# Performance work log

Measured on AMD Instinct MI355X. Metric: run time of the kernel, lower is better.

The kernel has to match this reference:

```python
import jax, jax.numpy as jnp
import numpy as np

ROPE_THETA = 10000.0

def _rope(x, offset=0):
    # x: [B, H, T, d]; lucidrains rotary_embedding_torch interleaved-pair convention
    d = x.shape[-1]
    T = x.shape[-2]
    inv_freq = 1.0 / (ROPE_THETA ** (jnp.arange(0, d, 2, dtype=jnp.float32) / d))  # [d/2]
    t = jnp.arange(offset, offset + T, dtype=jnp.float32)
    freqs = t[:, None] * inv_freq[None, :]                 # [T, d/2]
    freqs = jnp.repeat(freqs, 2, axis=-1)                  # [T, d] (each freq duplicated for its pair)
    cos = jnp.cos(freqs).astype(x.dtype)
    sin = jnp.sin(freqs).astype(x.dtype)
    xr = x.reshape(*x.shape[:-1], d // 2, 2)
    x1, x2 = xr[..., 0], xr[..., 1]
    rot = jnp.stack([-x2, x1], axis=-1).reshape(x.shape)   # rotate_half, interleaved
    return x * cos + rot * sin


def setup_inputs() -> dict:
    key = jax.random.key(0)
    ks = jax.random.split(key, 5)
    B, T, C = 8, 1024, 1024
    s = 0.02
    x = jax.random.normal(ks[0], (B, T, C), dtype=jnp.float32)
    ipw = jax.random.normal(ks[1], (3 * C, C), dtype=jnp.float32) * s
    ipb = jax.random.normal(ks[2], (3 * C,), dtype=jnp.float32) * s
    opw = jax.random.normal(ks[3], (C, C), dtype=jnp.float32) * s
    opb = jax.random.normal(ks[4], (C,), dtype=jnp.float32) * s
    # bool mask, True = blocked (original code inverts before SDPA) -> causal
    causal_block = ~jnp.tril(jnp.ones((T, T), dtype=bool))
    attn_mask = causal_block[None, None, :, :]             # [1,1,T,T]
    return {"x": x, "ipw": ipw, "ipb": ipb, "opw": opw, "opb": opb,
            "attn_mask": attn_mask}


def reference(x, ipw, ipb, opw, opb, attn_mask):
    B, T, C = x.shape
    n_head = 16
    hd = C // n_head
    qkv = x @ ipw.T + ipb                                  # [B,T,3C]
    q, k, v = jnp.split(qkv, 3, axis=-1)
    def heads(z):
        return z.reshape(B, T, n_head, hd).transpose(0, 2, 1, 3)  # [B,H,T,hd]
    q, k, v = heads(q), heads(k), heads(v)
    q = _rope(q)
    k = _rope(k)
    scores = jnp.einsum('bhqd,bhkd->bhqk', q, k) / jnp.sqrt(jnp.asarray(hd, x.dtype))
    # attn_mask True = blocked; mask slice [FULL_T-T:FULL_T, :FULL_T] is the full mask here
    scores = jnp.where(attn_mask, jnp.asarray(-1e9, x.dtype), scores)
    attn = jax.nn.softmax(scores, axis=-1)
    y = jnp.einsum('bhqk,bhkd->bhqd', attn, v)             # [B,H,T,hd]
    y = y.transpose(0, 2, 1, 3).reshape(B, T, C)
    return y @ opw.T + opb
```

## Files before the change

### kernel.cpp

```cpp
#include <hip/hip_runtime.h>
#include <stdint.h>


typedef __bf16 bf16x8 __attribute__((ext_vector_type(8)));
typedef float f32x4 __attribute__((ext_vector_type(4)));
typedef __attribute__((address_space(1))) unsigned int as1_u32;
typedef __attribute__((address_space(3))) unsigned int as3_u32;

#define MFMA16(a, b, c) __builtin_amdgcn_mfma_f32_16x16x32_bf16((a), (b), (c), 0, 0, 0)

static __device__ __forceinline__ unsigned short f2bf(float f) {
    union { float f; unsigned u; } x; x.f = f;
    return (unsigned short)((x.u + 0x7fffu + ((x.u >> 16) & 1u)) >> 16);
}
static __device__ __forceinline__ float bf2f(unsigned short u) {
    union { unsigned u; float f; } x; x.u = ((unsigned)u) << 16;
    return x.f;
}
static __device__ __forceinline__ bf16x8 ld_bf16x8(const void* p) {
    return *(const bf16x8*)p;
}
static __device__ __forceinline__ unsigned cvtpk(float lo, float hi) {
    unsigned r;
    asm("v_cvt_pk_bf16_f32 %0, %1, %2" : "=v"(r) : "v"(lo), "v"(hi));
    return r;
}

__global__ void cast_f32_bf16(const float* __restrict__ in,
                              unsigned short* __restrict__ out, int n8) {
    int i = blockIdx.x * blockDim.x + threadIdx.x;
    if (i >= n8) return;
    float4 a = ((const float4*)in)[2 * i];
    float4 b = ((const float4*)in)[2 * i + 1];
    union { unsigned short us[8]; uint4 v; } o;
    o.us[0] = f2bf(a.x); o.us[1] = f2bf(a.y); o.us[2] = f2bf(a.z); o.us[3] = f2bf(a.w);
    o.us[4] = f2bf(b.x); o.us[5] = f2bf(b.y); o.us[6] = f2bf(b.z); o.us[7] = f2bf(b.w);
    ((uint4*)out)[i] = o.v;
}

__global__ void rope_table(float* __restrict__ ct, float* __restrict__ st) {
    int idx = blockIdx.x * blockDim.x + threadIdx.x;
    if (idx >= 1024 * 32) return;
    int t = idx >> 5, i = idx & 31;
    float inv = powf(10000.0f, -(float)(2 * i) * (1.0f / 64.0f));
    float f = (float)t * inv;
    ct[idx] = cosf(f);
    st[idx] = sinf(f);
}

template <int NC, bool OUT_BF16>
__global__ __launch_bounds__(256) void gemm_bt(const unsigned short* __restrict__ A,
                                               const unsigned short* __restrict__ W,
                                               const float* __restrict__ bias,
                                               void* __restrict__ Cout, int K) {
    __shared__ __attribute__((aligned(16))) unsigned short As[128 * 32];
    __shared__ __attribute__((aligned(16))) unsigned short Bs[128 * 32];

    constexpr int NT = NC / 128;
    int nwg = gridDim.x;
    int bid = blockIdx.x;
    int lg = (bid & 7) * (nwg >> 3) + (bid >> 3);
    int tm = lg / NT, tn = lg % NT;
    int m0 = tm * 128, n0 = tn * 128;

    int tid = threadIdx.x;
    int w = tid >> 6, l = tid & 63;
    int lr = l & 15, g = l >> 4;
    int ldsb = __builtin_amdgcn_readfirstlane(w * 512);

    int c0 = tid, c1 = tid + 256;
    const unsigned short* A0 = A + (size_t)(m0 + (c0 >> 2)) * K + (c0 & 3) * 8;
    const unsigned short* A1 = A + (size_t)(m0 + (c1 >> 2)) * K + (c1 & 3) * 8;
    const unsigned short* W0 = W + (size_t)(n0 + (c0 >> 2)) * K + (c0 & 3) * 8;
    const unsigned short* W1 = W + (size_t)(n0 + (c1 >> 2)) * K + (c1 & 3) * 8;

    f32x4 acc[4][4] = {};
    int wr = (w >> 1) * 64, wc = (w & 1) * 64;

    for (int k0 = 0; k0 < K; k0 += 32) {
        __syncthreads();
        __builtin_amdgcn_global_load_lds((const as1_u32*)(A0 + k0), (as3_u32*)(As + ldsb), 16, 0, 0);
        __builtin_amdgcn_global_load_lds((const as1_u32*)(A1 + k0), (as3_u32*)(As + 2048 + ldsb), 16, 0, 0);
        __builtin_amdgcn_global_load_lds((const as1_u32*)(W0 + k0), (as3_u32*)(Bs + ldsb), 16, 0, 0);
        __builtin_amdgcn_global_load_lds((const as1_u32*)(W1 + k0), (as3_u32*)(Bs + 2048 + ldsb), 16, 0, 0);
        __syncthreads();

        bf16x8 a[4], b[4];
#pragma unroll
        for (int i = 0; i < 4; ++i) a[i] = ld_bf16x8(As + (wr + i * 16 + lr) * 32 + g * 8);
#pragma unroll
        for (int j = 0; j < 4; ++j) b[j] = ld_bf16x8(Bs + (wc + j * 16 + lr) * 32 + g * 8);
#pragma unroll
        for (int i = 0; i < 4; ++i)
#pragma unroll
            for (int j = 0; j < 4; ++j) acc[i][j] = MFMA16(a[i], b[j], acc[i][j]);
    }

    int g4 = g * 4;
#pragma unroll
    for (int j = 0; j < 4; ++j) {
        int col = n0 + wc + j * 16 + lr;
        float bv = bias[col];
#pragma unroll
        for (int i = 0; i < 4; ++i) {
#pragma unroll
            for (int r = 0; r < 4; ++r) {
                int row = m0 + wr + i * 16 + g4 + r;
                float v = acc[i][j][r] + bv;
                if (OUT_BF16)
                    ((unsigned short*)Cout)[(size_t)row * NC + col] = f2bf(v);
                else
                    ((float*)Cout)[(size_t)row * NC + col] = v;
            }
        }
    }
}

__global__ void rope_reshape(const unsigned short* __restrict__ qkv,
                             const float* __restrict__ ct, const float* __restrict__ st,
                             unsigned short* __restrict__ Qh,
                             unsigned short* __restrict__ Kh) {
    int idx = blockIdx.x * blockDim.x + threadIdx.x;
    if (idx >= 8192 * 256) return;
    int row = idx >> 8;
    int col = (idx & 255) * 8;
    int sec = col >> 10;
    int wi = col & 1023;
    int h = wi >> 6, d = wi & 63;
    int t = row & 1023;

    uint4 raw = *(const uint4*)(qkv + (size_t)row * 3072 + col);
    size_t obase = ((size_t)((row >> 10) * 16 + h) * 1024 + t) * 64 + d;

    union { uint4 v; unsigned short us[8]; } u; u.v = raw;
    float x[8];
#pragma unroll
    for (int i = 0; i < 8; ++i) x[i] = bf2f(u.us[i]);
    float scale = (sec == 0) ? 0.125f : 1.0f;
    union { uint4 v; unsigned short us[8]; } o;
#pragma unroll
    for (int p = 0; p < 4; ++p) {
        int fi = t * 32 + (d >> 1) + p;
        float c = ct[fi], s = st[fi];
        float e0 = (x[2 * p] * c - x[2 * p + 1] * s) * scale;
        float e1 = (x[2 * p + 1] * c + x[2 * p] * s) * scale;
        o.us[2 * p] = f2bf(e0);
        o.us[2 * p + 1] = f2bf(e1);
    }
    unsigned short* dst = (sec == 0) ? Qh : Kh;
    *(uint4*)(dst + obase) = o.v;
}

__global__ __launch_bounds__(256) void transpose_v(const unsigned short* __restrict__ qkv,
                                                   unsigned short* __restrict__ Vt) {
    __shared__ unsigned short Ts[64 * 67];
    int bid = blockIdx.x;
    int bh = bid >> 4, tt = bid & 15;
    int b = bh >> 4, h = bh & 15;
    int t0 = tt * 64;
    int tid = threadIdx.x;
#pragma unroll
    for (int cc = 0; cc < 2; ++cc) {
        int c = tid + cc * 256;
        int trow = c >> 3, d8 = (c & 7) * 8;
        uint4 v = *(const uint4*)(qkv + (size_t)(b * 1024 + t0 + trow) * 3072 + 2048 + h * 64 + d8);
        union { uint4 v; unsigned short us[8]; } u; u.v = v;
#pragma unroll
        for (int i = 0; i < 8; ++i) Ts[trow * 67 + d8 + i] = u.us[i];
    }
    __syncthreads();
#pragma unroll
    for (int cc = 0; cc < 2; ++cc) {
        int c = tid + cc * 256;
        int drow = c >> 3, t8 = (c & 7) * 8;
        union { uint4 v; unsigned short us[8]; } u;
#pragma unroll
        for (int i = 0; i < 8; ++i) u.us[i] = Ts[(t8 + i) * 67 + drow];
        *(uint4*)(Vt + (size_t)bh * 65536 + (size_t)drow * 1024 + t0 + t8) = u.v;
    }
}

__device__ __forceinline__ void attn_tile(const unsigned short* Ks, const unsigned short* Vs,
                                          bf16x8 q0f, bf16x8 q1f, f32x4 (&y)[4],
                                          float& rm, float& rl,
                                          int lr, int g, bool diag, int wq) {
    const char* kc = (const char*)Ks;
    const char* vc = (const char*)Vs;
    int l7 = lr & 7;
    int kof0 = lr * 128 + ((g ^ l7) << 4);
    int kof1 = lr * 128 + (((g + 4) ^ l7) << 4);
    f32x4 s[4];
#pragma unroll
    for (int nt = 0; nt < 4; ++nt) {
        bf16x8 kf0 = ld_bf16x8(kc + nt * 2048 + kof0);
        bf16x8 kf1 = ld_bf16x8(kc + nt * 2048 + kof1);
        f32x4 z = {};
        z = MFMA16(kf0, q0f, z);
        z = MFMA16(kf1, q1f, z);
        s[nt] = z;
    }
    if (diag) {
#pragma unroll
        for (int nt = 0; nt < 4; ++nt)
#pragma unroll
            for (int r = 0; r < 4; ++r)
                if (nt * 16 + g * 4 + r > wq + lr) s[nt][r] = -3e38f;
    }
    float tm;
    {
        f32x4 m4;
#pragma unroll
        for (int r = 0; r < 4; ++r) m4[r] = fmaxf(fmaxf(s[0][r], s[1][r]), fmaxf(s[2][r], s[3][r]));
        tm = fmaxf(fmaxf(m4[0], m4[1]), fmaxf(m4[2], m4[3]));
    }
    tm = fmaxf(tm, __shfl_xor(tm, 16));
    tm = fmaxf(tm, __shfl_xor(tm, 32));
    float nm = fmaxf(rm, tm);
    float alpha = __expf(rm - nm);
    rm = nm;
    float ts = 0.f;
#pragma unroll
    for (int nt = 0; nt < 4; ++nt)
#pragma unroll
        for (int r = 0; r < 4; ++r) { float pv = __expf(s[nt][r] - nm); s[nt][r] = pv; ts += pv; }
    ts += __shfl_xor(ts, 16);
    ts += __shfl_xor(ts, 32);
    rl = rl * alpha + ts;
#pragma unroll
    for (int nt = 0; nt < 4; ++nt) y[nt] *= alpha;
    union { unsigned u[4]; bf16x8 v; } pf0, pf1;
    pf0.u[0] = cvtpk(s[0][0], s[0][1]); pf0.u[1] = cvtpk(s[0][2], s[0][3]);
    pf0.u[2] = cvtpk(s[1][0], s[1][1]); pf0.u[3] = cvtpk(s[1][2], s[1][3]);
    pf1.u[0] = cvtpk(s[2][0], s[2][1]); pf1.u[1] = cvtpk(s[2][2], s[2][3]);
    pf1.u[2] = cvtpk(s[3][0], s[3][1]); pf1.u[3] = cvtpk(s[3][2], s[3][3]);
    int s0 = g >> 1, h8 = (g & 1) * 8;
    int vo0 = lr * 128 + h8 + (((s0 + 0) ^ l7) << 4);
    int vo1 = lr * 128 + h8 + (((s0 + 2) ^ l7) << 4);
    int vo2 = lr * 128 + h8 + (((s0 + 4) ^ l7) << 4);
    int vo3 = lr * 128 + h8 + (((s0 + 6) ^ l7) << 4);
#pragma unroll
    for (int nt = 0; nt < 4; ++nt) {
        union { uint2 u2[2]; bf16x8 v; } vf;
        vf.u2[0] = *(const uint2*)(vc + nt * 2048 + vo0);
        vf.u2[1] = *(const uint2*)(vc + nt * 2048 + vo1);
        y[nt] = MFMA16(vf.v, pf0.v, y[nt]);
        union { uint2 u2[2]; bf16x8 v; } vg;
        vg.u2[0] = *(const uint2*)(vc + nt * 2048 + vo2);
        vg.u2[1] = *(const uint2*)(vc + nt * 2048 + vo3);
        y[nt] = MFMA16(vg.v, pf1.v, y[nt]);
    }
}

__device__ __forceinline__ void attn_epilogue(unsigned short* smem, unsigned short* __restrict__ Yb,
                                              f32x4 (&y)[4], float rl, int qtile,
                                              int b, int hh, int w, int lr, int g, int tid) {
    __syncthreads();
    float inv = 1.0f / rl;
    char* ep = (char*)smem;
#pragma unroll
    for (int nt = 0; nt < 4; ++nt) {
        uint2 pr;
        pr.x = cvtpk(y[nt][0] * inv, y[nt][1] * inv);
        pr.y = cvtpk(y[nt][2] * inv, y[nt][3] * inv);
        *(uint2*)(ep + (w * 16 + lr) * 144 + (nt * 16 + g * 4) * 2) = pr;
    }
    __syncthreads();
    int q = tid >> 2, dc = (tid & 3) * 16;
    uint4 u0 = *(const uint4*)(ep + q * 144 + dc * 2);
    uint4 u1 = *(const uint4*)(ep + q * 144 + dc * 2 + 16);
    size_t orow = ((size_t)(b * 1024 + qtile * 64 + q)) * 1024 + hh * 64 + dc;
    *(uint4*)(Yb + orow) = u0;
    *(uint4*)(Yb + orow + 8) = u1;
}

__global__ __launch_bounds__(256) void attn_fwd(const unsigned short* __restrict__ Qh,
                                                const unsigned short* __restrict__ Kh,
                                                const unsigned short* __restrict__ Vt,
                                                unsigned short* __restrict__ Yb) {
    __shared__ __attribute__((aligned(16))) unsigned short smem[8192];
    unsigned short* Ks = smem;
    unsigned short* Vs = smem + 4096;

    int bid = blockIdx.x;
    int lg = (bid & 7) * 128 + (bid >> 3);
    int bh = lg >> 3, p = lg & 7;
    int qa = p, qb = 15 - p;

    int tid = threadIdx.x, w = tid >> 6, l = tid & 63;
    int lr = l & 15, g = l >> 4;
    int ldsb = __builtin_amdgcn_readfirstlane(w * 512);

    size_t bh64 = (size_t)bh * 65536;
    const unsigned short* qbase = Qh + bh64 + (size_t)(w * 16 + lr) * 64 + g * 8;
    bf16x8 qA0 = ld_bf16x8(qbase + qa * 4096);
    bf16x8 qA1 = ld_bf16x8(qbase + qa * 4096 + 32);
    bf16x8 qB0 = ld_bf16x8(qbase + qb * 4096);
    bf16x8 qB1 = ld_bf16x8(qbase + qb * 4096 + 32);

    f32x4 yA[4] = {}, yB[4] = {};
    float mA = -3e38f, lA = 0.f, mB = -3e38f, lB = 0.f;

    int c0 = tid, c1 = tid + 256;
    const unsigned short* K0 = Kh + bh64 + (c0 >> 3) * 64 + ((c0 ^ (c0 >> 3)) & 7) * 8;
    const unsigned short* K1 = Kh + bh64 + (c1 >> 3) * 64 + ((c1 ^ (c1 >> 3)) & 7) * 8;
    const unsigned short* V0 = Vt + bh64 + (c0 >> 3) * 1024 + ((c0 ^ (c0 >> 3)) & 7) * 8;
    const unsigned short* V1 = Vt + bh64 + (c1 >> 3) * 1024 + ((c1 ^ (c1 >> 3)) & 7) * 8;

    for (int t = 0; t <= qb; ++t) {
        __syncthreads();
        __builtin_amdgcn_global_load_lds((const as1_u32*)(K0 + t * 4096), (as3_u32*)(Ks + ldsb), 16, 0, 0);
        __builtin_amdgcn_global_load_lds((const as1_u32*)(K1 + t * 4096), (as3_u32*)(Ks + 2048 + ldsb), 16, 0, 0);
        __builtin_amdgcn_global_load_lds((const as1_u32*)(V0 + t * 64), (as3_u32*)(Vs + ldsb), 16, 0, 0);
        __builtin_amdgcn_global_load_lds((const as1_u32*)(V1 + t * 64), (as3_u32*)(Vs + 2048 + ldsb), 16, 0, 0);
        __syncthreads();

        if (t <= qa)
            attn_tile(Ks, Vs, qA0, qA1, yA, mA, lA, lr, g, t == qa, w * 16);
        attn_tile(Ks, Vs, qB0, qB1, yB, mB, lB, lr, g, t == qb, w * 16);
    }

    int b = bh >> 4, hh = bh & 15;
    attn_epilogue(smem, Yb, yA, lA, qa, b, hh, w, lr, g, tid);
    attn_epilogue(smem, Yb, yB, lB, qb, b, hh, w, lr, g, tid);
}

extern "C" void kernel_launch(void* const* d_in, const int* in_sizes, int n_in,
                              void* d_out, int out_size, void* d_ws, size_t ws_size,
                              hipStream_t stream) {
    const float* x = (const float*)d_in[0];
    const float* ipw = (const float*)d_in[1];
    const float* ipb = (const float*)d_in[2];
    const float* opw = (const float*)d_in[3];
    const float* opb = (const float*)d_in[4];

    char* ws = (char*)d_ws;
    unsigned short* xb   = (unsigned short*)(ws);
    unsigned short* wqkv = (unsigned short*)(ws + 16777216);
    unsigned short* wo   = (unsigned short*)(ws + 23068672);
    float* ct            = (float*)(ws + 25165824);
    float* st            = (float*)(ws + 25296896);
    unsigned short* qkvb = (unsigned short*)(ws + 25427968);
    unsigned short* Qh   = (unsigned short*)(ws + 75759616);
    unsigned short* Kh   = (unsigned short*)(ws + 92536832);
    unsigned short* Vt   = (unsigned short*)(ws + 109314048);
    unsigned short* yb   = (unsigned short*)(ws + 126091264);

    cast_f32_bf16<<<4096, 256, 0, stream>>>(x, xb, 1048576);
    cast_f32_bf16<<<1536, 256, 0, stream>>>(ipw, wqkv, 393216);
    cast_f32_bf16<<<512, 256, 0, stream>>>(opw, wo, 131072);
    rope_table<<<128, 256, 0, stream>>>(ct, st);

    gemm_bt<3072, true><<<1536, 256, 0, stream>>>(xb, wqkv, ipb, qkvb, 1024);
    rope_reshape<<<8192, 256, 0, stream>>>(qkvb, ct, st, Qh, Kh);
    transpose_v<<<2048, 256, 0, stream>>>(qkvb, Vt);
    attn_fwd<<<1024, 256, 0, stream>>>(Qh, Kh, Vt, yb);
    gemm_bt<1024, false><<<512, 256, 0, stream>>>(yb, wo, opb, d_out, 1024);
}
```

Before: 285.8 us.

## Replace QKV projection GEMM with 256x256-tile, 8-wave, 4-stage pipelined kernel

Swaps the 128x128 tiled QKV GEMM for a new kernel using 256x256 output tiles, 512 threads, and a 4-deep LDS ring buffer filled via direct global-to-LDS loads with an XOR-swizzled layout. Each K step is split into two phases that interleave the A and B prefetches with MFMA bursts, using setprio and explicit vmcnt waits. The goal is more data reuse per tile and better overlap of memory with matrix math. In exchange it uses 128 KB of LDS per block, a large accumulator set, and fewer workgroups (384), so occupancy and tail balance could suffer.

```diff
diff --git a/kernel.cpp b/kernel.cpp
--- a/kernel.cpp
+++ b/kernel.cpp
@@ -46,6 +46,116 @@
     float f = (float)t * inv;
     ct[idx] = cosf(f);
     st[idx] = sinf(f);
+}
+
+__global__ __launch_bounds__(512, 2) void gemm1_8ph(const unsigned short* __restrict__ A,
+                                                    const unsigned short* __restrict__ W,
+                                                    const float* __restrict__ bias,
+                                                    unsigned short* __restrict__ Cout) {
+    __shared__ __attribute__((aligned(16))) char lds[131072];
+    constexpr int NH = 32;
+    constexpr int NTN = 12;
+
+    int nwg = gridDim.x;
+    int bid = blockIdx.x;
+    int lg = (bid & 7) * (nwg >> 3) + (bid >> 3);
+    int tm = lg / NTN, tn = lg % NTN;
+    int m0 = tm * 256, n0 = tn * 256;
+
+    int tid = threadIdx.x;
+    int w = tid >> 6, l = tid & 63;
+    int lr = l & 15, g = l >> 4;
+    int wm = w >> 2, wn = w & 3;
+    int ldsb = __builtin_amdgcn_readfirstlane(w * 1024);
+
+    auto srcoff = [](int c) {
+        int row = c >> 3;
+        int sl = (c & 7) ^ (row & 7);
+        int rg = (row << 1) | (sl >> 2);
+        int cg = (sl & 3) * 8;
+        return rg * 1024 + cg;
+    };
+    int c0 = tid, c1 = tid + 512;
+    const unsigned short* pA0 = A + (size_t)m0 * 1024 + srcoff(c0);
+    const unsigned short* pA1 = A + (size_t)m0 * 1024 + srcoff(c1);
+    const unsigned short* pB0 = W + (size_t)n0 * 1024 + srcoff(c0);
+    const unsigned short* pB1 = W + (size_t)n0 * 1024 + srcoff(c1);
+
+    int lr2 = lr >> 1;
+    int sst16 = ((((lr & 1) << 2) + g) ^ lr2) << 4;
+    int aBase = (wm * 64 + lr2) * 128 + sst16;
+    int bBase = (wn * 32 + lr2) * 128 + sst16;
+
+    f32x4 acc[8][4] = {};
+
+    for (int js = 0; js < 3; ++js) {
+        char* Ad = lds + js * 16384;
+        char* Bd = lds + 65536 + js * 16384;
+        __builtin_amdgcn_global_load_lds((const as1_u32*)(pA0 + js * 32), (as3_u32*)(Ad + ldsb), 16, 0, 0);
+        __builtin_amdgcn_global_load_lds((const as1_u32*)(pA1 + js * 32), (as3_u32*)(Ad + 8192 + ldsb), 16, 0, 0);
+        __builtin_amdgcn_global_load_lds((const as1_u32*)(pB0 + js * 32), (as3_u32*)(Bd + ldsb), 16, 0, 0);
+        __builtin_amdgcn_global_load_lds((const as1_u32*)(pB1 + js * 32), (as3_u32*)(Bd + 8192 + ldsb), 16, 0, 0);
+    }
+    asm volatile("s_waitcnt vmcnt(8)" ::: "memory");
+    __builtin_amdgcn_s_barrier();
+
+#pragma unroll 4
+    for (int j = 0; j < NH; ++j) {
+        const char* Asl = lds + (j & 3) * 16384;
+        const char* Bsl = lds + 65536 + (j & 3) * 16384;
+        int js = j + 3;
+        char* Ad = lds + (js & 3) * 16384;
+        char* Bd = lds + 65536 + (js & 3) * 16384;
+        bf16x8 aa[4], bb[4];
+
+#pragma unroll
+        for (int fn = 0; fn < 4; ++fn) bb[fn] = ld_bf16x8(Bsl + bBase + fn * 1024);
+#pragma unroll
+        for (int fm = 0; fm < 4; ++fm) aa[fm] = ld_bf16x8(Asl + aBase + fm * 1024);
+        if (js < NH) {
+            __builtin_amdgcn_global_load_lds((const as1_u32*)(pA0 + js * 32), (as3_u32*)(Ad + ldsb), 16, 0, 0);
+            __builtin_amdgcn_global_load_lds((const as1_u32*)(pA1 + js * 32), (as3_u32*)(Ad + 8192 + ldsb), 16, 0, 0);
+        }
+        __builtin_amdgcn_s_barrier();
+        __builtin_amdgcn_s_setprio(1);
+#pragma unroll
+        for (int fm = 0; fm < 4; ++fm)
+#pragma unroll
+            for (int fn = 0; fn < 4; ++fn) acc[fm][fn] = MFMA16(aa[fm], bb[fn], acc[fm][fn]);
+        __builtin_amdgcn_s_setprio(0);
+        __builtin_amdgcn_s_barrier();
+
+#pragma unroll
+        for (int fm = 0; fm < 4; ++fm) aa[fm] = ld_bf16x8(Asl + aBase + (fm + 4) * 1024);
+        if (js < NH) {
+            __builtin_amdgcn_global_load_lds((const as1_u32*)(pB0 + js * 32), (as3_u32*)(Bd + ldsb), 16, 0, 0);
+            __builtin_amdgcn_global_load_lds((const as1_u32*)(pB1 + js * 32), (as3_u32*)(Bd + 8192 + ldsb), 16, 0, 0);
+        }
+        __builtin_amdgcn_s_barrier();
+        __builtin_amdgcn_s_setprio(1);
+#pragma unroll
+        for (int fm = 0; fm < 4; ++fm)
+#pragma unroll
+            for (int fn = 0; fn < 4; ++fn) acc[fm + 4][fn] = MFMA16(aa[fm], bb[fn], acc[fm + 4][fn]);
+        __builtin_amdgcn_s_setprio(0);
+        if (j + 3 < NH)      asm volatile("s_waitcnt vmcnt(8)" ::: "memory");
+        else if (j + 2 < NH) asm volatile("s_waitcnt vmcnt(4)" ::: "memory");
+        else if (j + 1 < NH) asm volatile("s_waitcnt vmcnt(0)" ::: "memory");
+        __builtin_amdgcn_s_barrier();
+    }
+
+#pragma unroll
+    for (int fn = 0; fn < 4; ++fn) {
+        int col = n0 + wn * 64 + fn * 16 + lr;
+        float bv = bias[col];
+#pragma unroll
+        for (int fm = 0; fm < 8; ++fm) {
+            int row = m0 + wm * 128 + fm * 16 + g * 4;
+#pragma unroll
+            for (int r = 0; r < 4; ++r)
+                Cout[(size_t)(row + r) * 3072 + col] = f2bf(acc[fm][fn][r] + bv);
+        }
+    }
 }
 
 template <int NC, bool OUT_BF16>
@@ -350,7 +460,7 @@
     cast_f32_bf16<<<512, 256, 0, stream>>>(opw, wo, 131072);
     rope_table<<<128, 256, 0, stream>>>(ct, st);
 
-    gemm_bt<3072, true><<<1536, 256, 0, stream>>>(xb, wqkv, ipb, qkvb, 1024);
+    gemm1_8ph<<<384, 512, 0, stream>>>(xb, wqkv, ipb, qkvb);
     rope_reshape<<<8192, 256, 0, stream>>>(qkvb, ct, st, Qh, Kh);
     transpose_v<<<2048, 256, 0, stream>>>(qkvb, Vt);
     attn_fwd<<<1024, 256, 0, stream>>>(Qh, Kh, Vt, yb);
```

After: 277.3 us. -3.0%, faster.

## Rewrite projection GEMMs with larger tiles, triple-buffered async LDS loads, swizzling

Applied to the files above, without the earlier changes.

Both projection GEMMs are replaced by specialized kernels with 512-thread blocks, larger 256x192 and 256x128 tiles, and a three-stage global-to-LDS pipeline with double-buffered register fragments. LDS layouts are XOR-swizzled to avoid bank conflicts. The QKV GEMM epilogue stages results through LDS for coalesced 16-byte stores. This targets the serialized load/sync/compute loop and the poor reuse of the old 128x128 kernel, at the cost of hardcoded shapes and more LDS per block, which limits occupancy.

```diff
diff --git a/kernel.cpp b/kernel.cpp
--- a/kernel.cpp
+++ b/kernel.cpp
@@ -8,6 +8,7 @@
 typedef __attribute__((address_space(3))) unsigned int as3_u32;
 
 #define MFMA16(a, b, c) __builtin_amdgcn_mfma_f32_16x16x32_bf16((a), (b), (c), 0, 0, 0)
+#define GLDS(src, dst) __builtin_amdgcn_global_load_lds((const as1_u32*)(src), (as3_u32*)(dst), 16, 0, 0)
 
 static __device__ __forceinline__ unsigned short f2bf(float f) {
     union { float f; unsigned u; } x; x.f = f;
@@ -48,70 +49,217 @@
     st[idx] = sinf(f);
 }
 
-template <int NC, bool OUT_BF16>
-__global__ __launch_bounds__(256) void gemm_bt(const unsigned short* __restrict__ A,
-                                               const unsigned short* __restrict__ W,
-                                               const float* __restrict__ bias,
-                                               void* __restrict__ Cout, int K) {
-    __shared__ __attribute__((aligned(16))) unsigned short As[128 * 32];
-    __shared__ __attribute__((aligned(16))) unsigned short Bs[128 * 32];
-
-    constexpr int NT = NC / 128;
+static __device__ __forceinline__ int srcoff(int c) {
+    int row = c >> 3;
+    int sl = (c & 7) ^ (row & 7);
+    return ((row << 1) | (sl >> 2)) * 1024 + (sl & 3) * 8;
+}
+
+__global__ __launch_bounds__(512, 2) void gemm1_p(const unsigned short* __restrict__ A,
+                                                  const unsigned short* __restrict__ W,
+                                                  const float* __restrict__ bias,
+                                                  unsigned short* __restrict__ Cout) {
+    __shared__ __attribute__((aligned(16))) char lds[86016];
+
     int nwg = gridDim.x;
     int bid = blockIdx.x;
     int lg = (bid & 7) * (nwg >> 3) + (bid >> 3);
-    int tm = lg / NT, tn = lg % NT;
-    int m0 = tm * 128, n0 = tn * 128;
-
-    int tid = threadIdx.x;
-    int w = tid >> 6, l = tid & 63;
-    int lr = l & 15, g = l >> 4;
-    int ldsb = __builtin_amdgcn_readfirstlane(w * 512);
-
-    int c0 = tid, c1 = tid + 256;
-    const unsigned short* A0 = A + (size_t)(m0 + (c0 >> 2)) * K + (c0 & 3) * 8;
-    const unsigned short* A1 = A + (size_t)(m0 + (c1 >> 2)) * K + (c1 & 3) * 8;
-    const unsigned short* W0 = W + (size_t)(n0 + (c0 >> 2)) * K + (c0 & 3) * 8;
-    const unsigned short* W1 = W + (size_t)(n0 + (c1 >> 2)) * K + (c1 & 3) * 8;
+    int tm = lg >> 4, tn = lg & 15;
+    int m0 = tm * 256, n0 = tn * 192;
+
+    int tid = threadIdx.x, w = tid >> 6, l = tid & 63;
+    int lr = l & 15, g = l >> 4, lr2 = lr >> 1;
+    int wm = w >> 1, wn = w & 1;
+    int ldsbA = __builtin_amdgcn_readfirstlane(w * 1024);
+    int ldsbB1 = __builtin_amdgcn_readfirstlane(w * 512) + 8192;
+
+    const unsigned short* pA0 = A + (size_t)m0 * 1024 + srcoff(tid);
+    const unsigned short* pA1 = A + (size_t)m0 * 1024 + srcoff(tid + 512);
+    const unsigned short* pB0 = W + (size_t)n0 * 1024 + srcoff(tid);
+    const unsigned short* pB1 = W + (size_t)n0 * 1024 + srcoff(512 + w * 32 + (l & 31));
+
+    int sst16 = ((((lr & 1) << 2) + g) ^ lr2) << 4;
+    int aBase = (wm * 32 + lr2) * 128 + sst16;
+    int bBase = (wn * 48 + lr2) * 128 + sst16;
+
+    f32x4 acc[4][6] = {};
+    bf16x8 af[2][4], bf[2][6];
+
+#pragma unroll
+    for (int s = 0; s < 3; ++s) {
+        char* Ad = lds + s * 16384;
+        char* Bd = lds + 49152 + s * 12288;
+        GLDS(pA0 + s * 32, Ad + ldsbA);
+        GLDS(pA1 + s * 32, Ad + 8192 + ldsbA);
+        GLDS(pB0 + s * 32, Bd + ldsbA);
+        if (l < 32) GLDS(pB1 + s * 32, Bd + ldsbB1);
+    }
+    asm volatile("s_waitcnt vmcnt(4)" ::: "memory");
+    __builtin_amdgcn_s_barrier();
+    __builtin_amdgcn_sched_barrier(0);
+    {
+        const char* As_ = lds;
+        const char* Bs_ = lds + 49152;
+#pragma unroll
+        for (int fm = 0; fm < 4; ++fm) af[0][fm] = ld_bf16x8(As_ + aBase + fm * 1024);
+#pragma unroll
+        for (int fn = 0; fn < 6; ++fn) bf[0][fn] = ld_bf16x8(Bs_ + bBase + fn * 1024);
+    }
+    asm volatile("s_waitcnt lgkmcnt(0)" ::: "memory");
+    __builtin_amdgcn_sched_barrier(0);
+
+#pragma unroll
+    for (int j = 0; j < 32; ++j) {
+        int cur = j & 1, nxt = cur ^ 1;
+        if (j < 31) {
+            const char* As_ = lds + ((j + 1) % 3) * 16384;
+            const char* Bs_ = lds + 49152 + ((j + 1) % 3) * 12288;
+#pragma unroll
+            for (int fm = 0; fm < 4; ++fm) af[nxt][fm] = ld_bf16x8(As_ + aBase + fm * 1024);
+#pragma unroll
+            for (int fn = 0; fn < 6; ++fn) bf[nxt][fn] = ld_bf16x8(Bs_ + bBase + fn * 1024);
+        }
+        if (j + 3 < 32) {
+            int ko = (j + 3) * 32;
+            char* Ad = lds + (j % 3) * 16384;
+            char* Bd = lds + 49152 + (j % 3) * 12288;
+            GLDS(pA0 + ko, Ad + ldsbA);
+            GLDS(pA1 + ko, Ad + 8192 + ldsbA);
+            GLDS(pB0 + ko, Bd + ldsbA);
+            if (l < 32) GLDS(pB1 + ko, Bd + ldsbB1);
+        }
+        __builtin_amdgcn_s_setprio(1);
+#pragma unroll
+        for (int fm = 0; fm < 4; ++fm)
+#pragma unroll
+            for (int fn = 0; fn < 6; ++fn) acc[fm][fn] = MFMA16(af[cur][fm], bf[cur][fn], acc[fm][fn]);
+        __builtin_amdgcn_s_setprio(0);
+        asm volatile("s_waitcnt lgkmcnt(0)" ::: "memory");
+        __builtin_amdgcn_sched_barrier(0);
+        if (j <= 28) asm volatile("s_waitcnt vmcnt(4)" ::: "memory");
+        else         asm volatile("s_waitcnt vmcnt(0)" ::: "memory");
+        __builtin_amdgcn_s_barrier();
+        __builtin_amdgcn_sched_barrier(0);
+    }
+
+    char* ep = lds + w * 3072;
+    float bv[6];
+#pragma unroll
+    for (int fn = 0; fn < 6; ++fn) bv[fn] = bias[n0 + wn * 96 + fn * 16 + lr];
+#pragma unroll
+    for (int fm = 0; fm < 4; ++fm) {
+#pragma unroll
+        for (int fn = 0; fn < 6; ++fn)
+#pragma unroll
+            for (int r = 0; r < 4; ++r)
+                *(unsigned short*)(ep + (g * 4 + r) * 192 + (((fn * 16 + lr) * 2) ^ (g << 4))) =
+                    f2bf(acc[fm][fn][r] + bv[fn]);
+        asm volatile("s_waitcnt lgkmcnt(0)" ::: "memory");
+        __builtin_amdgcn_sched_barrier(0);
+#pragma unroll
+        for (int i = 0; i < 3; ++i) {
+            int c = l + 64 * i;
+            int row = c / 12, ch = c - row * 12;
+            int swz = (row & 12) << 2;
+            uint4 v = *(const uint4*)(ep + row * 192 + ((ch * 16) ^ swz));
+            *(uint4*)(Cout + (size_t)(m0 + wm * 64 + fm * 16 + row) * 3072 + (n0 + wn * 96 + ch * 8)) = v;
+        }
+    }
+}
+
+__global__ __launch_bounds__(512, 2) void gemm2_p(const unsigned short* __restrict__ A,
+                                                  const unsigned short* __restrict__ W,
+                                                  const float* __restrict__ bias,
+                                                  float* __restrict__ Cout) {
+    __shared__ __attribute__((aligned(16))) char lds[73728];
+
+    int nwg = gridDim.x;
+    int bid = blockIdx.x;
+    int lg = (bid & 7) * (nwg >> 3) + (bid >> 3);
+    int tm = lg >> 3, tn = lg & 7;
+    int m0 = tm * 256, n0 = tn * 128;
+
+    int tid = threadIdx.x, w = tid >> 6, l = tid & 63;
+    int lr = l & 15, g = l >> 4, lr2 = lr >> 1;
+    int wm = w >> 1, wn = w & 1;
+    int ldsbA = __builtin_amdgcn_readfirstlane(w * 1024);
+
+    const unsigned short* pA0 = A + (size_t)m0 * 1024 + srcoff(tid);
+    const unsigned short* pA1 = A + (size_t)m0 * 1024 + srcoff(tid + 512);
+    const unsigned short* pB0 = W + (size_t)n0 * 1024 + srcoff(tid);
+
+    int sst16 = ((((lr & 1) << 2) + g) ^ lr2) << 4;
+    int aBase = (wm * 32 + lr2) * 128 + sst16;
+    int bBase = (wn * 32 + lr2) * 128 + sst16;
 
     f32x4 acc[4][4] = {};
-    int wr = (w >> 1) * 64, wc = (w & 1) * 64;
-
-    for (int k0 = 0; k0 < K; k0 += 32) {
-        __syncthreads();
-        __builtin_amdgcn_global_load_lds((const as1_u32*)(A0 + k0), (as3_u32*)(As + ldsb), 16, 0, 0);
-        __builtin_amdgcn_global_load_lds((const as1_u32*)(A1 + k0), (as3_u32*)(As + 2048 + ldsb), 16, 0, 0);
-        __builtin_amdgcn_global_load_lds((const as1_u32*)(W0 + k0), (as3_u32*)(Bs + ldsb), 16, 0, 0);
-        __builtin_amdgcn_global_load_lds((const as1_u32*)(W1 + k0), (as3_u32*)(Bs + 2048 + ldsb), 16, 0, 0);
-        __syncthreads();
-
-        bf16x8 a[4], b[4];
-#pragma unroll
-        for (int i = 0; i < 4; ++i) a[i] = ld_bf16x8(As + (wr + i * 16 + lr) * 32 + g * 8);
-#pragma unroll
-        for (int j = 0; j < 4; ++j) b[j] = ld_bf16x8(Bs + (wc + j * 16 + lr) * 32 + g * 8);
-#pragma unroll
-        for (int i = 0; i < 4; ++i)
-#pragma unroll
-            for (int j = 0; j < 4; ++j) acc[i][j] = MFMA16(a[i], b[j], acc[i][j]);
-    }
-
-    int g4 = g * 4;
-#pragma unroll
-    for (int j = 0; j < 4; ++j) {
-        int col = n0 + wc + j * 16 + lr;
+    bf16x8 af[2][4], bf[2][4];
+
+#pragma unroll
+    for (int s = 0; s < 3; ++s) {
+        char* Ad = lds + s * 16384;
+        char* Bd = lds + 49152 + s * 8192;
+        GLDS(pA0 + s * 32, Ad + ldsbA);
+        GLDS(pA1 + s * 32, Ad + 8192 + ldsbA);
+        GLDS(pB0 + s * 32, Bd + ldsbA);
+    }
+    asm volatile("s_waitcnt vmcnt(3)" ::: "memory");
+    __builtin_amdgcn_s_barrier();
+    __builtin_amdgcn_sched_barrier(0);
+    {
+        const char* As_ = lds;
+        const char* Bs_ = lds + 49152;
+#pragma unroll
+        for (int fm = 0; fm < 4; ++fm) af[0][fm] = ld_bf16x8(As_ + aBase + fm * 1024);
+#pragma unroll
+        for (int fn = 0; fn < 4; ++fn) bf[0][fn] = ld_bf16x8(Bs_ + bBase + fn * 1024);
+    }
+    asm volatile("s_waitcnt lgkmcnt(0)" ::: "memory");
+    __builtin_amdgcn_sched_barrier(0);
+
+#pragma unroll
+    for (int j = 0; j < 32; ++j) {
+        int cur = j & 1, nxt = cur ^ 1;
+        if (j < 31) {
+            const char* As_ = lds + ((j + 1) % 3) * 16384;
+            const char* Bs_ = lds + 49152 + ((j + 1) % 3) * 8192;
+#pragma unroll
+            for (int fm = 0; fm < 4; ++fm) af[nxt][fm] = ld_bf16x8(As_ + aBase + fm * 1024);
+#pragma unroll
+            for (int fn = 0; fn < 4; ++fn) bf[nxt][fn] = ld_bf16x8(Bs_ + bBase + fn * 1024);
+        }
+        if (j + 3 < 32) {
+            int ko = (j + 3) * 32;
+            char* Ad = lds + (j % 3) * 16384;
+            char* Bd = lds + 49152 + (j % 3) * 8192;
+            GLDS(pA0 + ko, Ad + ldsbA);
+            GLDS(pA1 + ko, Ad + 8192 + ldsbA);
+            GLDS(pB0 + ko, Bd + ldsbA);
+        }
+        __builtin_amdgcn_s_setprio(1);
+#pragma unroll
+        for (int fm = 0; fm < 4; ++fm)
+#pragma unroll
+            for (int fn = 0; fn < 4; ++fn) acc[fm][fn] = MFMA16(af[cur][fm], bf[cur][fn], acc[fm][fn]);
+        __builtin_amdgcn_s_setprio(0);
+        asm volatile("s_waitcnt lgkmcnt(0)" ::: "memory");
+        __builtin_amdgcn_sched_barrier(0);
+        if (j <= 28) asm volatile("s_waitcnt vmcnt(3)" ::: "memory");
+        else         asm volatile("s_waitcnt vmcnt(0)" ::: "memory");
+        __builtin_amdgcn_s_barrier();
+        __builtin_amdgcn_sched_barrier(0);
+    }
+
+#pragma unroll
+    for (int fn = 0; fn < 4; ++fn) {
+        int col = n0 + wn * 64 + fn * 16 + lr;
         float bv = bias[col];
 #pragma unroll
-        for (int i = 0; i < 4; ++i) {
-#pragma unroll
-            for (int r = 0; r < 4; ++r) {
-                int row = m0 + wr + i * 16 + g4 + r;
-                float v = acc[i][j][r] + bv;
-                if (OUT_BF16)
-                    ((unsigned short*)Cout)[(size_t)row * NC + col] = f2bf(v);
-                else
-                    ((float*)Cout)[(size_t)row * NC + col] = v;
-            }
+        for (int fm = 0; fm < 4; ++fm) {
+            int row = m0 + wm * 64 + fm * 16 + g * 4;
+#pragma unroll
+            for (int r = 0; r < 4; ++r)
+                Cout[(size_t)(row + r) * 1024 + col] = acc[fm][fn][r] + bv;
         }
     }
 }
@@ -350,9 +498,9 @@
     cast_f32_bf16<<<512, 256, 0, stream>>>(opw, wo, 131072);
     rope_table<<<128, 256, 0, stream>>>(ct, st);
 
-    gemm_bt<3072, true><<<1536, 256, 0, stream>>>(xb, wqkv, ipb, qkvb, 1024);
+    gemm1_p<<<512, 512, 0, stream>>>(xb, wqkv, ipb, qkvb);
     rope_reshape<<<8192, 256, 0, stream>>>(qkvb, ct, st, Qh, Kh);
     transpose_v<<<2048, 256, 0, stream>>>(qkvb, Vt);
     attn_fwd<<<1024, 256, 0, stream>>>(Qh, Kh, Vt, yb);
-    gemm_bt<1024, false><<<512, 256, 0, stream>>>(yb, wo, opb, d_out, 1024);
-}
+    gemm2_p<<<256, 512, 0, stream>>>(yb, wo, opb, (float*)d_out);
+}
```

After: 259.5 us. -9.2%, faster.
